# Performance work log

Measured on AMD Instinct MI355X. Metric: run time of the kernel, lower is better.

The kernel has to match this reference:

```python
import jax, jax.numpy as jnp
import numpy as np

N = 100000
E = 1600000
IN_DIM, HID, OUT = 512, 256, 32
EPS = 1e-16  # matches PyG softmax denominator epsilon


def gat_layer(xp, a_src, a_dst, src, dst, n_nodes):
    """Single-head GAT propagate with sigmoid + segment softmax, scatter-add.
    xp: [N, C] projected features; a_src/a_dst: [N] per-node attention logits;
    src/dst: [E] edge endpoints (message flows src -> dst)."""
    alpha = jax.nn.sigmoid(a_src[src] + a_dst[dst])  # [E]
    m = jax.ops.segment_max(alpha, dst, num_segments=n_nodes)  # [N]
    ex = jnp.exp(alpha - m[dst])
    denom = jax.ops.segment_sum(ex, dst, num_segments=n_nodes)  # [N]
    a = ex / (denom[dst] + EPS)  # [E]
    msg = xp[src] * a[:, None]  # [E, C]
    return jax.ops.segment_sum(msg, dst, num_segments=n_nodes)  # [N, C]


def setup_inputs() -> dict:
    key = jax.random.key(0)
    k1, k2, k3, k4, k5, k6, k7, k8 = jax.random.split(key, 8)
    features = jax.random.normal(k1, (N, IN_DIM), dtype=jnp.float32)
    edge_index = jax.random.randint(k2, (2, E), 0, N, dtype=jnp.int64)
    g = 1.414
    W1 = jax.random.normal(k3, (IN_DIM, HID), dtype=jnp.float32) * (g * np.sqrt(2.0 / (IN_DIM + HID)))
    W2 = jax.random.normal(k4, (HID, OUT), dtype=jnp.float32) * (g * np.sqrt(2.0 / (HID + OUT)))
    att_src1 = jax.random.normal(k5, (HID,), dtype=jnp.float32) * (g * np.sqrt(2.0 / (1 + HID)))
    att_dst1 = jax.random.normal(k6, (HID,), dtype=jnp.float32) * (g * np.sqrt(2.0 / (1 + HID)))
    return {"features": features, "edge_index": edge_index, "W1": W1, "W2": W2,
            "att_src1": att_src1, "att_dst1": att_dst1}


def reference(features, edge_index, W1, W2, att_src1, att_dst1):
    src, dst = edge_index[0], edge_index[1]
    # conv1 (with attention)
    xp1 = features @ W1  # [N, HID]
    a_src = xp1 @ att_src1  # [N]
    a_dst = xp1 @ att_dst1  # [N]
    h1 = jax.nn.elu(gat_layer(xp1, a_src, a_dst, src, dst, N))
    # conv2 (attention=False -> plain linear, mean over 1 head)
    h2 = h1 @ W2  # [N, OUT]
    # conv3: weights tied to W2^T, attention tied to conv1's per-node logits
    xp3 = h2 @ W2.T  # [N, HID]
    h3 = jax.nn.elu(gat_layer(xp3, a_src, a_dst, src, dst, N))
    # conv4 (attention=False): weights tied to W1^T
    h4 = h3 @ W1.T  # [N, IN_DIM]
    return h2, h4
```

## Files before the change

kernel.cpp:

```cpp
#include <hip/hip_runtime.h>
#include <cstdint>
#include <cstddef>

#define INDIM 512
#define HIDD  256
#define OUTD  32
#define PCH   4096
#define SHIFT 9
#define SLABN 512

typedef __attribute__((ext_vector_type(4))) float f32x4;
typedef __attribute__((ext_vector_type(8))) short bf16x8;

static inline __device__ float b2f(unsigned short u) {
  union { float f; unsigned int i; } v; v.i = ((unsigned int)u) << 16; return v.f;
}
static inline __device__ unsigned short f2b(float f) {
  union { float f; unsigned int i; } v; v.f = f;
  unsigned int x = v.i;
  x += 0x7fffu + ((x >> 16) & 1u);
  return (unsigned short)(x >> 16);
}

static inline __device__ float edgew(float x) {
  float al = 1.f / (1.f + __expf(-x));
  return __expf(al);
}

static __device__ __forceinline__ void gld16(const unsigned short* g, unsigned short* l) {
  __builtin_amdgcn_global_load_lds(
      (const __attribute__((address_space(1))) void*)g,
      (__attribute__((address_space(3))) void*)l, 16, 0, 0);
}

__global__ __launch_bounds__(256) void probe_kernel(
    const unsigned int* __restrict__ feat, const unsigned int* __restrict__ eidx,
    int* __restrict__ flags)
{
  int t = threadIdx.x;
  __shared__ int cnt, oddnz;
  if (t == 0) { cnt = 0; oddnz = 0; }
  __syncthreads();
  unsigned int w = feat[t];
  unsigned short lo = (unsigned short)(w & 0xFFFFu);
  int e = (lo >> 7) & 0xFF;
  int plausible = ((lo & 0x7FFF) == 0) || (e >= 0x60 && e <= 0x9F);
  atomicAdd(&cnt, plausible);
  if (t & 1) { if (eidx[t] != 0u) atomicAdd(&oddnz, 1); }
  __syncthreads();
  if (t == 0) { flags[0] = (cnt >= 192) ? 1 : 0; flags[1] = (oddnz == 0) ? 1 : 0; }
}

__global__ __launch_bounds__(256) void cnt_kernel(
    const unsigned int* __restrict__ eidx, int* __restrict__ bcnt,
    int E, const int* __restrict__ flags)
{
  __shared__ int hist[256];
  int t = threadIdx.x;
  hist[t] = 0;
  __syncthreads();
  int e0 = blockIdx.x * PCH;
  const int i64 = flags[1];
  for (int i = t; i < PCH; i += 256) {
    int e = e0 + i; if (e >= E) break;
    int d = i64 ? (int)eidx[2 * ((size_t)E + e)] : (int)eidx[(size_t)E + e];
    atomicAdd(&hist[d >> SHIFT], 1);
  }
  __syncthreads();
  bcnt[blockIdx.x * 256 + t] = hist[t];
}

__global__ __launch_bounds__(256) void bscan_kernel(
    int* __restrict__ bcnt, int* __restrict__ slabOff, int npb)
{
  __shared__ int wsum[4];
  int t = threadIdx.x, lane = t & 63, wv = t >> 6;
  int run = 0;
  for (int b = 0; b < npb; ++b) {
    int v = bcnt[b * 256 + t];
    bcnt[b * 256 + t] = run;
    run += v;
  }
  int inc = run;
#pragma unroll
  for (int o = 1; o < 64; o <<= 1) {
    int u = __shfl_up(inc, o);
    if (lane >= o) inc += u;
  }
  if (lane == 63) wsum[wv] = inc;
  __syncthreads();
  if (t < 4) {
    int v = wsum[t], s = v;
#pragma unroll
    for (int o = 1; o < 4; o <<= 1) {
      int u = __shfl_up(s, o);
      if (t >= o) s += u;
    }
    wsum[t] = s - v;
  }
  __syncthreads();
  int exc = wsum[wv] + inc - run;
  slabOff[t] = exc;
  if (t == 255) slabOff[256] = exc + run;
}

__global__ __launch_bounds__(256) void scat_kernel(
    const unsigned int* __restrict__ eidx, const int* __restrict__ bcnt,
    const int* __restrict__ slabOff, uint2* __restrict__ part,
    int E, const int* __restrict__ flags)
{
  __shared__ int cur[256];
  int t = threadIdx.x;
  cur[t] = slabOff[t] + bcnt[blockIdx.x * 256 + t];
  __syncthreads();
  int e0 = blockIdx.x * PCH;
  const int i64 = flags[1];
  for (int i = t; i < PCH; i += 256) {
    int e = e0 + i; if (e >= E) break;
    int s, d;
    if (i64) { s = (int)eidx[2 * (size_t)e]; d = (int)eidx[2 * ((size_t)E + e)]; }
    else     { s = (int)eidx[e];             d = (int)eidx[(size_t)E + e]; }
    int pos = atomicAdd(&cur[d >> SHIFT], 1);
    part[pos] = make_uint2((unsigned)s, (unsigned)d);
  }
}

__global__ __launch_bounds__(256) void slabcsr_kernel(
    const uint2* __restrict__ part, const int* __restrict__ slabOff,
    int* __restrict__ offs, int* __restrict__ srcP, int N, int nslab)
{
  __shared__ int deg[SLABN];
  __shared__ int wsum[4];
  int sl = blockIdx.x, t = threadIdx.x;
  int n0 = sl << SHIFT;
  int nn = N - n0; if (nn > SLABN) nn = SLABN;
  int s0 = slabOff[sl], s1 = slabOff[sl + 1];
  for (int i = t; i < SLABN; i += 256) deg[i] = 0;
  __syncthreads();
  for (int i = s0 + t; i < s1; i += 256)
    atomicAdd(&deg[(int)part[i].y - n0], 1);
  __syncthreads();
  int bi = t * 2;
  int l0 = deg[bi], l1 = deg[bi + 1];
  int s = l0 + l1;
  int ws = s;
#pragma unroll
  for (int o = 1; o < 64; o <<= 1) {
    int u = __shfl_up(ws, o);
    if ((t & 63) >= o) ws += u;
  }
  if ((t & 63) == 63) wsum[t >> 6] = ws;
  __syncthreads();
  if (t < 4) {
    int v = wsum[t], inc = v;
#pragma unroll
    for (int o = 1; o < 4; o <<= 1) {
      int u = __shfl_up(inc, o);
      if (t >= o) inc += u;
    }
    wsum[t] = inc - v;
  }
  __syncthreads();
  int run = wsum[t >> 6] + (ws - s);
  deg[bi] = run;
  if (bi < nn) offs[n0 + bi] = s0 + run;
  run += l0;
  deg[bi + 1] = run;
  if (bi + 1 < nn) offs[n0 + bi + 1] = s0 + run;
  __syncthreads();
  for (int i = s0 + t; i < s1; i += 256) {
    uint2 p = part[i];
    int pos = s0 + atomicAdd(&deg[(int)p.y - n0], 1);
    srcP[pos] = (int)p.x;
  }
  if (sl == nslab - 1 && t == 0) offs[N] = s1;
}

static inline __device__ float ldadapt(const void* p, size_t i, int isbf) {
  return isbf ? b2f(((const unsigned short*)p)[i]) : ((const float*)p)[i];
}

__global__ __launch_bounds__(256) void prep_weights(
    const void* __restrict__ W1, const void* __restrict__ W2,
    const void* __restrict__ aS, const void* __restrict__ aD,
    unsigned short* __restrict__ W1b, unsigned short* __restrict__ W1tb,
    float* __restrict__ W2f, unsigned short* __restrict__ W2b64,
    float* __restrict__ atS, float* __restrict__ atD,
    const int* __restrict__ flags)
{
  const int fb = flags[0];
  int i = blockIdx.x * 256 + threadIdx.x;
  if (i < INDIM * HIDD) {
    int r = i >> 8, c = i & 255;
    float w0 = ldadapt(W1, i, fb);
    unsigned short wb = f2b(w0);
    W1b[i] = wb;
    W1tb[c * INDIM + r] = wb;
  }
  if (i < HIDD * OUTD) {
    int r = i >> 5, c = i & 31;
    float w0 = ldadapt(W2, i, fb);
    W2f[i] = w0;
    W2b64[r * 64 + c] = f2b(w0);
    W2b64[r * 64 + 32 + c] = 0;
  }
  if (i < HIDD) { atS[i] = ldadapt(aS, i, fb); atD[i] = ldadapt(aD, i, fb); }
}

template<int AMODE, int OUTMODE, int EPI>
__global__ __launch_bounds__(512, 4) void gemm_nt2(
    const void* __restrict__ Av, const unsigned short* __restrict__ Bt,
    unsigned short* __restrict__ Cb, void* __restrict__ Out, size_t outOff,
    const int* __restrict__ flags, int M, int Nn, int K)
{
  __shared__ unsigned short Als[128 * 64];
  __shared__ unsigned short Bls[256 * 64];
  const int tid = threadIdx.x, lane = tid & 63, wid = tid >> 6;
  const int wr = wid >> 2, wc = wid & 3;
  const int rowBase = blockIdx.y * 128, colBase = blockIdx.x * 256;
  const int fb = flags[0];

  const int srow = (lane >> 3), sg = lane & 7;
  const int sgx = sg ^ srow;

  f32x4 acc[4][4] = {};

  for (int kt = 0; kt < K; kt += 64) {
    if (AMODE == 1 && !fb) {
      const float* Af = (const float*)Av;
#pragma unroll
      for (int i = 0; i < 2; ++i) {
        int row = wid * 16 + i * 8 + srow;
        int gr = rowBase + row; if (gr > M - 1) gr = M - 1;
        const float* sp = Af + (size_t)gr * K + kt + sg * 8;
        float4 lo = *(const float4*)sp;
        float4 hi = *(const float4*)(sp + 4);
        union { unsigned short us[8]; int4 v; } cv;
        cv.us[0] = f2b(lo.x); cv.us[1] = f2b(lo.y); cv.us[2] = f2b(lo.z); cv.us[3] = f2b(lo.w);
        cv.us[4] = f2b(hi.x); cv.us[5] = f2b(hi.y); cv.us[6] = f2b(hi.z); cv.us[7] = f2b(hi.w);
        *(int4*)(Als + row * 64 + (sgx << 3)) = cv.v;
      }
    } else {
      const unsigned short* Ab = (const unsigned short*)Av;
#pragma unroll
      for (int i = 0; i < 2; ++i) {
        int row = wid * 16 + i * 8 + srow;
        int gr = rowBase + row;
        if (AMODE == 1 && gr > M - 1) gr = M - 1;
        gld16(Ab + (size_t)gr * K + kt + (sgx << 3), Als + (wid * 2 + i) * 512);
      }
    }
#pragma unroll
    for (int i = 0; i < 4; ++i) {
      int row = wid * 32 + i * 8 + srow;
      gld16(Bt + (size_t)(colBase + row) * K + kt + (sgx << 3), Bls + (wid * 4 + i) * 512);
    }
    __syncthreads();

    bf16x8 af[4], bfr[4];
#pragma unroll
    for (int ks = 0; ks < 2; ++ks) {
      int gl = ks * 4 + (lane >> 4);
      int gx = gl ^ (lane & 7);
#pragma unroll
      for (int mi = 0; mi < 4; ++mi) {
        int row = wr * 64 + mi * 16 + (lane & 15);
        af[mi] = *(const bf16x8*)(Als + row * 64 + (gx << 3));
      }
#pragma unroll
      for (int ni = 0; ni < 4; ++ni) {
        int row = wc * 64 + ni * 16 + (lane & 15);
        bfr[ni] = *(const bf16x8*)(Bls + row * 64 + (gx << 3));
      }
#pragma unroll
      for (int mi = 0; mi < 4; ++mi)
#pragma unroll
        for (int ni = 0; ni < 4; ++ni)
          acc[mi][ni] = __builtin_amdgcn_mfma_f32_16x16x32_bf16(af[mi], bfr[ni], acc[mi][ni], 0, 0, 0);
    }
    __syncthreads();
  }

#pragma unroll
  for (int mi = 0; mi < 4; ++mi) {
    int r0 = rowBase + wr * 64 + mi * 16 + (lane >> 4) * 4;
#pragma unroll
    for (int ni = 0; ni < 4; ++ni) {
      int c = colBase + wc * 64 + ni * 16 + (lane & 15);
#pragma unroll
      for (int v = 0; v < 4; ++v) {
        int r = r0 + v;
        if (r < M) {
          size_t idx = (size_t)r * Nn + c;
          float x = acc[mi][ni][v];
          if (EPI) x = x > 0.f ? x : expm1f(x);
          if (OUTMODE == 0) Cb[idx] = f2b(x);
          else {
            if (fb) ((unsigned short*)Out)[outOff + idx] = f2b(x);
            else    ((float*)Out)[outOff + idx] = x;
          }
        }
      }
    }
  }
}

__global__ __launch_bounds__(256) void rowdots(
    const unsigned short* __restrict__ P, const float* __restrict__ atS,
    const float* __restrict__ atD,
    float* __restrict__ asrc, float* __restrict__ adst, int N)
{
  int wave = threadIdx.x >> 6, lane = threadIdx.x & 63;
  int node = blockIdx.x * 4 + wave;
  if (node >= N) return;
  ushort4 u = *(const ushort4*)(P + (size_t)node * HIDD + lane * 4);
  float4 v = make_float4(b2f(u.x), b2f(u.y), b2f(u.z), b2f(u.w));
  float4 s = *(const float4*)(atS + lane * 4);
  float4 d = *(const float4*)(atD + lane * 4);
  float s1 = v.x * s.x + v.y * s.y + v.z * s.z + v.w * s.w;
  float s2 = v.x * d.x + v.y * d.y + v.z * d.z + v.w * d.w;
#pragma unroll
  for (int off = 32; off; off >>= 1) {
    s1 += __shfl_down(s1, off);
    s2 += __shfl_down(s2, off);
  }
  if (lane == 0) { asrc[node] = s1; adst[node] = s2; }
}

__global__ __launch_bounds__(256) void agg_elu2(
    const unsigned short* __restrict__ xp,
    const float* __restrict__ asrc, const float* __restrict__ adst,
    const int* __restrict__ srcP, const int* __restrict__ offs,
    unsigned short* __restrict__ hout, int N)
{
  __shared__ int   sS[4][64];
  __shared__ float sW[4][64];
  int wid = threadIdx.x >> 6, lane = threadIdx.x & 63;
  int node = blockIdx.x * 4 + wid;
  if (node >= N) return;
  const float ad = adst[node];
  int s0 = offs[node], s1 = offs[node + 1];
  float a0 = 0.f, a1 = 0.f, a2 = 0.f, a3 = 0.f, den = 0.f;
  for (int base = s0; base < s1; base += 64) {
    int cnt = s1 - base; if (cnt > 64) cnt = 64;
    if (lane < cnt) {
      int sv = srcP[base + lane];
      sS[wid][lane] = sv;
      sW[wid][lane] = edgew(asrc[sv] + ad);
    }
    asm volatile("s_waitcnt lgkmcnt(0)" ::: "memory");
    int j = 0;
    for (; j + 16 <= cnt; j += 16) {
      ushort4 u[16];
#pragma unroll
      for (int q = 0; q < 16; ++q)
        u[q] = *(const ushort4*)(xp + (size_t)sS[wid][j + q] * HIDD + lane * 4);
#pragma unroll
      for (int q = 0; q < 16; ++q) {
        float wv = sW[wid][j + q];
        den += wv;
        a0 += wv * b2f(u[q].x); a1 += wv * b2f(u[q].y);
        a2 += wv * b2f(u[q].z); a3 += wv * b2f(u[q].w);
      }
    }
    for (; j + 8 <= cnt; j += 8) {
      ushort4 u[8];
#pragma unroll
      for (int q = 0; q < 8; ++q)
        u[q] = *(const ushort4*)(xp + (size_t)sS[wid][j + q] * HIDD + lane * 4);
#pragma unroll
      for (int q = 0; q < 8; ++q) {
        float wv = sW[wid][j + q];
        den += wv;
        a0 += wv * b2f(u[q].x); a1 += wv * b2f(u[q].y);
        a2 += wv * b2f(u[q].z); a3 += wv * b2f(u[q].w);
      }
    }
    for (; j < cnt; ++j) {
      int   sv = sS[wid][j];
      float wv = sW[wid][j];
      den += wv;
      ushort4 u = *(const ushort4*)(xp + (size_t)sv * HIDD + lane * 4);
      a0 += wv * b2f(u.x); a1 += wv * b2f(u.y); a2 += wv * b2f(u.z); a3 += wv * b2f(u.w);
    }
  }
  float inv = 1.f / (den + 1e-16f);
  float r0 = a0 * inv, r1 = a1 * inv, r2 = a2 * inv, r3 = a3 * inv;
  r0 = r0 > 0.f ? r0 : expm1f(r0);
  r1 = r1 > 0.f ? r1 : expm1f(r1);
  r2 = r2 > 0.f ? r2 : expm1f(r2);
  r3 = r3 > 0.f ? r3 : expm1f(r3);
  ushort4 o; o.x = f2b(r0); o.y = f2b(r1); o.z = f2b(r2); o.w = f2b(r3);
  *(ushort4*)(hout + (size_t)node * HIDD + lane * 4) = o;
}

__global__ __launch_bounds__(256) void gemm_h2(
    const unsigned short* __restrict__ H1, const float* __restrict__ W2f,
    void* __restrict__ Out, unsigned short* __restrict__ h2b,
    const int* __restrict__ flags, int M)
{
  const int fb = flags[0];
  __shared__ float Bs[HIDD][33];
  __shared__ float As[8][HIDD];
  int tid = threadIdx.x;
  int tx = tid & 31, ty = tid >> 5;
  int row0 = blockIdx.x * 8;
#pragma unroll
  for (int j = 0; j < 8; ++j) {
    int idx4 = tid + 256 * j;
    float4 v = *(const float4*)(W2f + idx4 * 4);
    int k = idx4 >> 3, c = (idx4 & 7) * 4;
    Bs[k][c] = v.x; Bs[k][c + 1] = v.y; Bs[k][c + 2] = v.z; Bs[k][c + 3] = v.w;
  }
  {
    int flat = tid * 8;
    int r = flat >> 8, k = flat & 255;
    int gr = row0 + r;
    if (gr < M) {
      ushort4 lo = *(const ushort4*)(H1 + (size_t)gr * HIDD + k);
      ushort4 hi = *(const ushort4*)(H1 + (size_t)gr * HIDD + k + 4);
      As[r][k] = b2f(lo.x); As[r][k + 1] = b2f(lo.y); As[r][k + 2] = b2f(lo.z); As[r][k + 3] = b2f(lo.w);
      As[r][k + 4] = b2f(hi.x); As[r][k + 5] = b2f(hi.y); As[r][k + 6] = b2f(hi.z); As[r][k + 7] = b2f(hi.w);
    } else {
#pragma unroll
      for (int q = 0; q < 8; ++q) As[r][k + q] = 0.f;
    }
  }
  __syncthreads();
  float acc = 0.f;
#pragma unroll 8
  for (int k = 0; k < HIDD; ++k) acc += As[ty][k] * Bs[k][tx];
  int row = row0 + ty;
  if (row < M) {
    size_t idx = (size_t)row * OUTD + tx;
    if (fb) ((unsigned short*)Out)[idx] = f2b(acc);
    else    ((float*)Out)[idx] = acc;
    h2b[idx] = f2b(acc);
  }
}

__global__ __launch_bounds__(256) void agg_small(
    const unsigned short* __restrict__ h2b,
    const float* __restrict__ asrc, const float* __restrict__ adst,
    const int* __restrict__ srcP, const int* __restrict__ offs,
    unsigned short* __restrict__ g2pad, int N)
{
  int wid = threadIdx.x >> 6, lane = threadIdx.x & 63;
  int node = blockIdx.x * 4 + wid;
  if (node >= N) return;
  int grp = lane >> 4, cl = lane & 15;
  const float ad = adst[node];
  int s0 = offs[node], s1 = offs[node + 1];
  float a0 = 0.f, a1 = 0.f, den = 0.f;
  for (int e = s0 + grp; e < s1; e += 4) {
    int   sv = srcP[e];
    float wv = edgew(asrc[sv] + ad);
    den += wv;
    ushort2 u = *(const ushort2*)(h2b + (size_t)sv * OUTD + cl * 2);
    a0 += wv * b2f(u.x);
    a1 += wv * b2f(u.y);
  }
  a0 += __shfl_xor(a0, 16); a0 += __shfl_xor(a0, 32);
  a1 += __shfl_xor(a1, 16); a1 += __shfl_xor(a1, 32);
  den += __shfl_xor(den, 16); den += __shfl_xor(den, 32);
  if (grp == 0) {
    float inv = 1.f / (den + 1e-16f);
    ushort2 o; o.x = f2b(a0 * inv); o.y = f2b(a1 * inv);
    *(ushort2*)(g2pad + (size_t)node * 64 + cl * 2) = o;
  } else if (grp == 1) {
    *(ushort2*)(g2pad + (size_t)node * 64 + 32 + cl * 2) = make_ushort2(0, 0);
  }
}

extern "C" void kernel_launch(void* const* d_in, const int* in_sizes, int n_in,
                              void* d_out, int out_size, void* d_ws, size_t ws_size,
                              hipStream_t stream)
{
  const void*         feat = d_in[0];
  const unsigned int* eidx = (const unsigned int*)d_in[1];
  const void*         W1   = d_in[2];
  const void*         W2   = d_in[3];
  const void*         aS   = d_in[4];
  const void*         aD   = d_in[5];

  const int N = in_sizes[0] / INDIM;
  const int E = in_sizes[1] / 2;
  const int M_pad = ((N + 127) / 128) * 128;
  const int nslab = (N + SLABN - 1) / SLABN;
  const int npb = (E + PCH - 1) / PCH;

  char* w = (char*)d_ws;
  auto alloc = [&](size_t bytes) -> char* {
    char* p = w; w += (bytes + 255) & ~(size_t)255; return p;
  };
  unsigned short* H     = (unsigned short*)alloc((size_t)M_pad * HIDD * 2);
  unsigned short* P     = (unsigned short*)alloc((size_t)M_pad * HIDD * 2);
  unsigned short* h2b   = (unsigned short*)alloc((size_t)N * OUTD * 2);
  unsigned short* g2pad = (unsigned short*)alloc((size_t)M_pad * 64 * 2);
  float* asrc = (float*)alloc((size_t)N * 4);
  float* adst = (float*)alloc((size_t)N * 4);
  int*   srcP = (int*)alloc((size_t)E * 4);
  uint2* part = (uint2*)alloc((size_t)E * 8);
  int*   offs = (int*)alloc((size_t)(N + 1) * 4);
  int*   bcnt = (int*)alloc((size_t)npb * 256 * 4);
  int*   slabOff = (int*)alloc(257 * 4);
  unsigned short* W1b   = (unsigned short*)alloc((size_t)INDIM * HIDD * 2);
  unsigned short* W1tb  = (unsigned short*)alloc((size_t)INDIM * HIDD * 2);
  unsigned short* W2b64 = (unsigned short*)alloc((size_t)HIDD * 64 * 2);
  float* W2f  = (float*)alloc((size_t)HIDD * OUTD * 4);
  float* atS  = (float*)alloc((size_t)HIDD * 4);
  float* atD  = (float*)alloc((size_t)HIDD * 4);
  int*   flags = (int*)alloc(64);

  probe_kernel<<<1, 256, 0, stream>>>((const unsigned int*)feat, eidx, flags);

  cnt_kernel<<<npb, 256, 0, stream>>>(eidx, bcnt, E, flags);
  bscan_kernel<<<1, 256, 0, stream>>>(bcnt, slabOff, npb);
  scat_kernel<<<npb, 256, 0, stream>>>(eidx, bcnt, slabOff, part, E, flags);
  slabcsr_kernel<<<nslab, 256, 0, stream>>>(part, slabOff, offs, srcP, N, nslab);

  prep_weights<<<512, 256, 0, stream>>>(W1, W2, aS, aD, W1b, W1tb, W2f, W2b64, atS, atD, flags);

  const int mb = (N + 127) / 128;

  gemm_nt2<1, 0, 0><<<dim3(1, mb), 512, 0, stream>>>(
      feat, W1tb, P, nullptr, 0, flags, N, HIDD, INDIM);

  rowdots<<<(N + 3) / 4, 256, 0, stream>>>(P, atS, atD, asrc, adst, N);

  agg_elu2<<<(N + 3) / 4, 256, 0, stream>>>(P, asrc, adst, srcP, offs, H, N);

  gemm_h2<<<(N + 7) / 8, 256, 0, stream>>>(H, W2f, d_out, h2b, flags, N);

  agg_small<<<(N + 3) / 4, 256, 0, stream>>>(h2b, asrc, adst, srcP, offs, g2pad, N);

  gemm_nt2<0, 0, 1><<<dim3(1, mb), 512, 0, stream>>>(
      g2pad, W2b64, H, nullptr, 0, flags, N, HIDD, 64);

  gemm_nt2<0, 1, 0><<<dim3(2, mb), 512, 0, stream>>>(
      H, W1b, nullptr, d_out, (size_t)N * OUTD, flags, N, INDIM, HIDD);
}
```

Baseline: 609.6 us.

## Fuse attention row-dots into first GEMM and W2^T projection into small aggregation

The per-node attention logits are now computed in the epilogue of the first projection GEMM by reducing accumulator fragments against the attention vectors through shuffles and shared-memory atomics, which removes the separate rowdots pass that re-read the projected features. The second aggregation kernel now also multiplies the aggregated 32-wide result by W2^T held in shared memory and applies ELU, writing the 256-wide hidden directly. This removes the padded intermediate buffer and a small-K GEMM launch. In exchange, each aggregation block loads a 32 KB transposed weight tile into LDS. It also relies on an inline waitcnt rather than a barrier to order the shared writes within a wave, and it does the projection in fp32 scalar FMAs instead of matrix instructions.

Measured after the change: 897.0 us. 47.1% more time.

```diff
diff --git a/kernel.cpp b/kernel.cpp
--- a/kernel.cpp
+++ b/kernel.cpp
@@ -184,7 +184,7 @@
     const void* __restrict__ W1, const void* __restrict__ W2,
     const void* __restrict__ aS, const void* __restrict__ aD,
     unsigned short* __restrict__ W1b, unsigned short* __restrict__ W1tb,
-    float* __restrict__ W2f, unsigned short* __restrict__ W2b64,
+    float* __restrict__ W2f,
     float* __restrict__ atS, float* __restrict__ atD,
     const int* __restrict__ flags)
 {
@@ -197,24 +197,21 @@
     W1b[i] = wb;
     W1tb[c * INDIM + r] = wb;
   }
-  if (i < HIDD * OUTD) {
-    int r = i >> 5, c = i & 31;
-    float w0 = ldadapt(W2, i, fb);
-    W2f[i] = w0;
-    W2b64[r * 64 + c] = f2b(w0);
-    W2b64[r * 64 + 32 + c] = 0;
-  }
+  if (i < HIDD * OUTD) W2f[i] = ldadapt(W2, i, fb);
   if (i < HIDD) { atS[i] = ldadapt(aS, i, fb); atD[i] = ldadapt(aD, i, fb); }
 }
 
-template<int AMODE, int OUTMODE, int EPI>
+template<int AMODE, int OUTMODE, int EPI, int DOTS>
 __global__ __launch_bounds__(512, 4) void gemm_nt2(
     const void* __restrict__ Av, const unsigned short* __restrict__ Bt,
     unsigned short* __restrict__ Cb, void* __restrict__ Out, size_t outOff,
+    const float* __restrict__ atS, const float* __restrict__ atD,
+    float* __restrict__ asrc, float* __restrict__ adst,
     const int* __restrict__ flags, int M, int Nn, int K)
 {
   __shared__ unsigned short Als[128 * 64];
   __shared__ unsigned short Bls[256 * 64];
+  __shared__ float sdot[2][128];
   const int tid = threadIdx.x, lane = tid & 63, wid = tid >> 6;
   const int wr = wid >> 2, wc = wid & 3;
   const int rowBase = blockIdx.y * 128, colBase = blockIdx.x * 256;
@@ -303,28 +300,44 @@
       }
     }
   }
-}
-
-__global__ __launch_bounds__(256) void rowdots(
-    const unsigned short* __restrict__ P, const float* __restrict__ atS,
-    const float* __restrict__ atD,
-    float* __restrict__ asrc, float* __restrict__ adst, int N)
-{
-  int wave = threadIdx.x >> 6, lane = threadIdx.x & 63;
-  int node = blockIdx.x * 4 + wave;
-  if (node >= N) return;
-  ushort4 u = *(const ushort4*)(P + (size_t)node * HIDD + lane * 4);
-  float4 v = make_float4(b2f(u.x), b2f(u.y), b2f(u.z), b2f(u.w));
-  float4 s = *(const float4*)(atS + lane * 4);
-  float4 d = *(const float4*)(atD + lane * 4);
-  float s1 = v.x * s.x + v.y * s.y + v.z * s.z + v.w * s.w;
-  float s2 = v.x * d.x + v.y * d.y + v.z * d.z + v.w * d.w;
-#pragma unroll
-  for (int off = 32; off; off >>= 1) {
-    s1 += __shfl_down(s1, off);
-    s2 += __shfl_down(s2, off);
-  }
-  if (lane == 0) { asrc[node] = s1; adst[node] = s2; }
+
+  if (DOTS) {
+    if (tid < 128) { sdot[0][tid] = 0.f; sdot[1][tid] = 0.f; }
+    __syncthreads();
+    float vS[4], vD[4];
+#pragma unroll
+    for (int ni = 0; ni < 4; ++ni) {
+      int c = colBase + wc * 64 + ni * 16 + (lane & 15);
+      vS[ni] = atS[c]; vD[ni] = atD[c];
+    }
+#pragma unroll
+    for (int mi = 0; mi < 4; ++mi) {
+#pragma unroll
+      for (int v = 0; v < 4; ++v) {
+        float ps = 0.f, pd = 0.f;
+#pragma unroll
+        for (int ni = 0; ni < 4; ++ni) {
+          ps += acc[mi][ni][v] * vS[ni];
+          pd += acc[mi][ni][v] * vD[ni];
+        }
+#pragma unroll
+        for (int off = 1; off < 16; off <<= 1) {
+          ps += __shfl_xor(ps, off);
+          pd += __shfl_xor(pd, off);
+        }
+        if ((lane & 15) == 0) {
+          int rl = wr * 64 + mi * 16 + (lane >> 4) * 4 + v;
+          atomicAdd(&sdot[0][rl], ps);
+          atomicAdd(&sdot[1][rl], pd);
+        }
+      }
+    }
+    __syncthreads();
+    if (tid < 128) {
+      int r = rowBase + tid;
+      if (r < M) { asrc[r] = sdot[0][tid]; adst[r] = sdot[1][tid]; }
+    }
+  }
 }
 
 __global__ __launch_bounds__(256) void agg_elu2(
@@ -439,13 +452,22 @@
   }
 }
 
-__global__ __launch_bounds__(256) void agg_small(
+__global__ __launch_bounds__(256) void agg_small2(
     const unsigned short* __restrict__ h2b,
     const float* __restrict__ asrc, const float* __restrict__ adst,
     const int* __restrict__ srcP, const int* __restrict__ offs,
-    unsigned short* __restrict__ g2pad, int N)
-{
-  int wid = threadIdx.x >> 6, lane = threadIdx.x & 63;
+    const float* __restrict__ W2f,
+    unsigned short* __restrict__ h3out, int N)
+{
+  __shared__ float W2T[32][256];
+  __shared__ float sg2[4][32];
+  int tid = threadIdx.x;
+  for (int i = tid; i < HIDD * OUTD; i += 256) {
+    int c = i >> 5, j = i & 31;
+    W2T[j][c] = W2f[i];
+  }
+  __syncthreads();
+  int wid = tid >> 6, lane = tid & 63;
   int node = blockIdx.x * 4 + wid;
   if (node >= N) return;
   int grp = lane >> 4, cl = lane & 15;
@@ -465,11 +487,23 @@
   den += __shfl_xor(den, 16); den += __shfl_xor(den, 32);
   if (grp == 0) {
     float inv = 1.f / (den + 1e-16f);
-    ushort2 o; o.x = f2b(a0 * inv); o.y = f2b(a1 * inv);
-    *(ushort2*)(g2pad + (size_t)node * 64 + cl * 2) = o;
-  } else if (grp == 1) {
-    *(ushort2*)(g2pad + (size_t)node * 64 + 32 + cl * 2) = make_ushort2(0, 0);
-  }
+    sg2[wid][cl * 2] = a0 * inv;
+    sg2[wid][cl * 2 + 1] = a1 * inv;
+  }
+  asm volatile("s_waitcnt lgkmcnt(0)" ::: "memory");
+  float o0 = 0.f, o1 = 0.f, o2 = 0.f, o3 = 0.f;
+#pragma unroll 8
+  for (int j = 0; j < 32; ++j) {
+    float g = sg2[wid][j];
+    float4 wv = *(const float4*)(&W2T[j][lane * 4]);
+    o0 += g * wv.x; o1 += g * wv.y; o2 += g * wv.z; o3 += g * wv.w;
+  }
+  o0 = o0 > 0.f ? o0 : expm1f(o0);
+  o1 = o1 > 0.f ? o1 : expm1f(o1);
+  o2 = o2 > 0.f ? o2 : expm1f(o2);
+  o3 = o3 > 0.f ? o3 : expm1f(o3);
+  ushort4 o; o.x = f2b(o0); o.y = f2b(o1); o.z = f2b(o2); o.w = f2b(o3);
+  *(ushort4*)(h3out + (size_t)node * HIDD + lane * 4) = o;
 }
 
 extern "C" void kernel_launch(void* const* d_in, const int* in_sizes, int n_in,
@@ -496,7 +530,6 @@
   unsigned short* H     = (unsigned short*)alloc((size_t)M_pad * HIDD * 2);
   unsigned short* P     = (unsigned short*)alloc((size_t)M_pad * HIDD * 2);
   unsigned short* h2b   = (unsigned short*)alloc((size_t)N * OUTD * 2);
-  unsigned short* g2pad = (unsigned short*)alloc((size_t)M_pad * 64 * 2);
   float* asrc = (float*)alloc((size_t)N * 4);
   float* adst = (float*)alloc((size_t)N * 4);
   int*   srcP = (int*)alloc((size_t)E * 4);
@@ -506,7 +539,6 @@
   int*   slabOff = (int*)alloc(257 * 4);
   unsigned short* W1b   = (unsigned short*)alloc((size_t)INDIM * HIDD * 2);
   unsigned short* W1tb  = (unsigned short*)alloc((size_t)INDIM * HIDD * 2);
-  unsigned short* W2b64 = (unsigned short*)alloc((size_t)HIDD * 64 * 2);
   float* W2f  = (float*)alloc((size_t)HIDD * OUTD * 4);
   float* atS  = (float*)alloc((size_t)HIDD * 4);
   float* atD  = (float*)alloc((size_t)HIDD * 4);
@@ -519,24 +551,20 @@
   scat_kernel<<<npb, 256, 0, stream>>>(eidx, bcnt, slabOff, part, E, flags);
   slabcsr_kernel<<<nslab, 256, 0, stream>>>(part, slabOff, offs, srcP, N, nslab);
 
-  prep_weights<<<512, 256, 0, stream>>>(W1, W2, aS, aD, W1b, W1tb, W2f, W2b64, atS, atD, flags);
+  prep_weights<<<512, 256, 0, stream>>>(W1, W2, aS, aD, W1b, W1tb, W2f, atS, atD, flags);
 
   const int mb = (N + 127) / 128;
 
-  gemm_nt2<1, 0, 0><<<dim3(1, mb), 512, 0, stream>>>(
-      feat, W1tb, P, nullptr, 0, flags, N, HIDD, INDIM);
-
-  rowdots<<<(N + 3) / 4, 256, 0, stream>>>(P, atS, atD, asrc, adst, N);
+  gemm_nt2<1, 0, 0, 1><<<dim3(1, mb), 512, 0, stream>>>(
+      feat, W1tb, P, nullptr, 0, atS, atD, asrc, adst, flags, N, HIDD, INDIM);
 
   agg_elu2<<<(N + 3) / 4, 256, 0, stream>>>(P, asrc, adst, srcP, offs, H, N);
 
   gemm_h2<<<(N + 7) / 8, 256, 0, stream>>>(H, W2f, d_out, h2b, flags, N);
 
-  agg_small<<<(N + 3) / 4, 256, 0, stream>>>(h2b, asrc, adst, srcP, offs, g2pad, N);
-
-  gemm_nt2<0, 0, 1><<<dim3(1, mb), 512, 0, stream>>>(
-      g2pad, W2b64, H, nullptr, 0, flags, N, HIDD, 64);
-
-  gemm_nt2<0, 1, 0><<<dim3(2, mb), 512, 0, stream>>>(
-      H, W1b, nullptr, d_out, (size_t)N * OUTD, flags, N, INDIM, HIDD);
-}
+  agg_small2<<<(N + 3) / 4, 256, 0, stream>>>(h2b, asrc, adst, srcP, offs, W2f, H, N);
+
+  gemm_nt2<0, 1, 0, 0><<<dim3(2, mb), 512, 0, stream>>>(
+      H, W1b, nullptr, d_out, (size_t)N * OUTD, nullptr, nullptr, nullptr, nullptr,
+      flags, N, INDIM, HIDD);
+}
```
